# Optimization experiments

Measured on AMD Instinct MI355X. Metric: run time of the kernel, lower is better.

## Reference

```python
import jax, jax.numpy as jnp
import numpy as np

B, N = 4, 65536
Z_DIM, HIDDEN, N_LAYERS = 64, 128, 4
PE_FREQS = 10
FEAT_RES = 16  # global_feat_res
IN_DIM = Z_DIM + 3 + 3 * 2 * PE_FREQS  # latent + pos-encoded coords


def setup_inputs() -> dict:
    key = jax.random.key(0)
    ks = jax.random.split(key, 4 + 2 * N_LAYERS)
    inp = {}
    # xyz in [-1,1]: used directly as grid_sample grid coordinates
    inp['xyz'] = jax.random.uniform(ks[0], (B, N, 3), jnp.float32, -1.0, 1.0)
    inp['local_latents'] = jax.random.normal(ks[1], (B, Z_DIM, FEAT_RES, FEAT_RES), jnp.float32)
    dims = [IN_DIM] + [HIDDEN] * N_LAYERS
    for i in range(N_LAYERS):
        inp[f'W{i}'] = jax.random.normal(ks[2 + i], (dims[i], dims[i + 1]), jnp.float32) / np.sqrt(dims[i]).astype(np.float32)
        inp[f'b{i}'] = jnp.zeros((dims[i + 1],), jnp.float32)
    inp['Wa'] = jax.random.normal(ks[2 + N_LAYERS], (HIDDEN, 1), jnp.float32) / np.sqrt(HIDDEN).astype(np.float32)
    inp['ba'] = jnp.zeros((1,), jnp.float32)
    return inp


def grid_sample_2d(img, grid):
    # torch F.grid_sample: bilinear, align_corners=False, padding_mode='zeros'
    # img [B,C,H,W], grid [B,Hg,Wg,2] in [-1,1], (x,y) order -> out [B,C,Hg,Wg]
    _, _, H, W = img.shape
    x = (grid[..., 0] + 1.0) * (W * 0.5) - 0.5
    y = (grid[..., 1] + 1.0) * (H * 0.5) - 0.5
    x0 = jnp.floor(x); y0 = jnp.floor(y)
    x1 = x0 + 1.0; y1 = y0 + 1.0

    def gather(ix, iy):
        valid = (ix >= 0) & (ix <= W - 1) & (iy >= 0) & (iy <= H - 1)
        ixc = jnp.clip(ix, 0, W - 1).astype(jnp.int32)
        iyc = jnp.clip(iy, 0, H - 1).astype(jnp.int32)
        v = jax.vmap(lambda im, yy, xx: im[:, yy, xx])(img, iyc, ixc)  # [B,C,Hg,Wg]
        return v * valid[:, None].astype(img.dtype)

    out = (gather(x0, y0) * ((x1 - x) * (y1 - y))[:, None]
           + gather(x0, y1) * ((x1 - x) * (y - y0))[:, None]
           + gather(x1, y0) * ((x - x0) * (y1 - y))[:, None]
           + gather(x1, y1) * ((x - x0) * (y - y0))[:, None])
    return out


def positional_encoding(x):
    # x [P,3] -> [P, 3 + 3*2*PE_FREQS]
    freqs = 2.0 ** jnp.arange(PE_FREQS, dtype=x.dtype)
    ang = x[..., None, :] * freqs[:, None]  # [P, L, 3]
    P = x.shape[0]
    return jnp.concatenate([x, jnp.sin(ang).reshape(P, -1), jnp.cos(ang).reshape(P, -1)], axis=-1)


def _forward(xyz, local_latents, Ws, bs, Wa, ba):
    xyz4 = xyz[:, None]  # [B, 1, N, 3] (forward's xyz.unsqueeze(1))
    # sample_local_latents: 4D latents -> grid = xyz[..., [0, 2]]
    grid = jnp.stack([xyz4[..., 0], xyz4[..., 2]], axis=-1)  # [B,1,N,2]
    samp = grid_sample_2d(local_latents, grid)               # [B,C,1,N]
    z = samp.transpose(0, 2, 3, 1).reshape(-1, Z_DIM)        # [B*N, C]
    # get_local_coordinates (preserve_y=True since latents are 4D)
    lc = (xyz4 + 1.0) * 0.5 * FEAT_RES
    lc = lc - jnp.round(lc - 0.5)  # round-half-to-even matches torch .round()
    lc = lc * 2.0 - 1.0
    coords = jnp.concatenate([lc[..., 0:1], xyz4[..., 1:2], lc[..., 2:3]], axis=-1).reshape(-1, 3)
    # local_generator MLP (viewdirs=None on alpha-only path)
    h = jnp.concatenate([z, positional_encoding(coords)], axis=-1)
    for W, b in zip(Ws, bs):
        h = jax.nn.relu(h @ W + b)
    alpha = h @ Wa + ba  # [B*N, 1], raw alpha (activation happens in volume render, not here)
    return alpha.reshape(xyz.shape[0], 1, -1)  # alpha.view(B, n_samples=1, samples_per_ray=N)


def reference(xyz, local_latents, W0, b0, W1, b1, W2, b2, W3, b3, Wa, ba):
    return _forward(xyz, local_latents, (W0, W1, W2, W3), (b0, b1, b2, b3), Wa, ba)
```

## Files before the change

kernel.cpp:

```cpp
#include <hip/hip_runtime.h>
#include <hip/hip_bf16.h>

typedef float f32x4 __attribute__((ext_vector_type(4)));
typedef short bf16x8 __attribute__((ext_vector_type(8)));

__device__ __forceinline__ unsigned pk2(float lo, float hi) {
  union { __hip_bfloat162 h2; unsigned u; } c;
  c.h2 = __float22bfloat162_rn(make_float2(lo, hi));
  return c.u;
}
__device__ __forceinline__ ushort f2bf1(float f) {
  union { __hip_bfloat16 h; ushort u; } c;
  c.h = __float2bfloat16(f);
  return c.u;
}
__device__ __forceinline__ float u2f(unsigned u) {
  union { unsigned u; float f; } c; c.u = u; return c.f;
}

__global__ void pack_all(const float* __restrict__ W0, const float* __restrict__ W1,
                         const float* __restrict__ W2, const float* __restrict__ W3,
                         const float* __restrict__ b0, const float* __restrict__ b1,
                         const float* __restrict__ b2, const float* __restrict__ b3,
                         const float* __restrict__ lat,
                         ushort* __restrict__ wpk, float* __restrict__ biasf,
                         ushort* __restrict__ latpk) {
  int t = blockIdx.x * 256 + threadIdx.x;
  if (t < 8192) {
    int lane = t & 63, kt = (t >> 6) & 3, jt = (t >> 8) & 7, layer = t >> 11;
    const float* W = layer == 0 ? W0 : layer == 1 ? W1 : layer == 2 ? W2 : W3;
    int K = (layer == 0) ? 127 : 128;
    int g = lane >> 4, r = lane & 15;
    bf16x8 pk;
#pragma unroll
    for (int i = 0; i < 8; i++) {
      int k = kt * 32 + 8 * g + i;
      pk[i] = (short)((k < K) ? f2bf1(W[k * 128 + jt * 16 + r]) : (ushort)0);
    }
    *(bf16x8*)(wpk + ((t >> 11) * 32 + (jt * 4 + kt)) * 512 + lane * 8) = pk;
  } else if (t < 16384) {
    int t2 = t - 8192;
    int g = t2 & 7, pix = (t2 >> 3) & 255, b = t2 >> 11;
    uint4 w;
    unsigned* wp = &w.x;
#pragma unroll
    for (int i = 0; i < 4; i++)
      wp[i] = pk2(lat[(b * 64 + 8 * g + 2 * i) * 256 + pix],
                  lat[(b * 64 + 8 * g + 2 * i + 1) * 256 + pix]);
    *(uint4*)((char*)latpk + b * 32768 + pix * 128 + ((16 * g) ^ ((pix & 7) << 4))) = w;
  } else if (t < 16896) {
    int t3 = t - 16384;
    int layer = t3 >> 7, j = t3 & 127;
    const float* b = layer == 0 ? b0 : layer == 1 ? b1 : layer == 2 ? b2 : b3;
    biasf[t3] = b[j];
  }
}

__global__ __launch_bounds__(256, 4) void scene_fwd(
    const float* __restrict__ xyz, const ushort* __restrict__ latpk,
    const ushort* __restrict__ wpk, const float* __restrict__ biasf,
    const float* __restrict__ wa, const float* __restrict__ ba,
    float* __restrict__ out) {
  __shared__ char smem[32768];
  const int tid = threadIdx.x;
  const int wave = tid >> 6, lane = tid & 63;
  const int g = lane >> 4, r = lane & 15;
  const int p0 = blockIdx.x * 128;
  const int batch = blockIdx.x >> 9;

  {
    uint4* dst = (uint4*)smem;
    const uint4* src = (const uint4*)((const char*)latpk + batch * 32768);
#pragma unroll
    for (int i = 0; i < 8; i++) dst[i * 256 + tid] = src[i * 256 + tid];
  }
  __syncthreads();

  const int t2 = tid & 127;
  const int p = p0 + t2;
  const float X = xyz[3 * p + 0], Y = xyz[3 * p + 1], Z = xyz[3 * p + 2];
  uint4 fr[8];
  if (tid < 128) {
    float gx = (X + 1.f) * 8.f - 0.5f;
    float gy = (Z + 1.f) * 8.f - 0.5f;
    float x0f = floorf(gx), y0f = floorf(gy);
    float fx = gx - x0f, fy = gy - y0f;
    int ix0 = (int)x0f, iy0 = (int)y0f;
    int ix1 = ix0 + 1, iy1 = iy0 + 1;
    float vx0 = (ix0 >= 0 && ix0 <= 15) ? 1.f : 0.f;
    float vx1 = (ix1 >= 0 && ix1 <= 15) ? 1.f : 0.f;
    float vy0 = (iy0 >= 0 && iy0 <= 15) ? 1.f : 0.f;
    float vy1 = (iy1 >= 0 && iy1 <= 15) ? 1.f : 0.f;
    int cx0 = min(max(ix0, 0), 15), cx1 = min(max(ix1, 0), 15);
    int cy0 = min(max(iy0, 0), 15), cy1 = min(max(iy1, 0), 15);
    float w00 = (1.f - fx) * (1.f - fy) * vx0 * vy0;
    float w01 = (1.f - fx) * fy * vx0 * vy1;
    float w10 = fx * (1.f - fy) * vx1 * vy0;
    float w11 = fx * fy * vx1 * vy1;
    int px00 = cy0 * 16 + cx0, px01 = cy1 * 16 + cx0;
    int px10 = cy0 * 16 + cx1, px11 = cy1 * 16 + cx1;
    int o00 = px00 * 128, s00 = (px00 & 7) << 4;
    int o01 = px01 * 128, s01 = (px01 & 7) << 4;
    int o10 = px10 * 128, s10 = (px10 & 7) << 4;
    int o11 = px11 * 128, s11 = (px11 & 7) << 4;
#pragma unroll
    for (int gr = 0; gr < 8; gr++) {
      const int off = 16 * gr;
      float f[8];
#pragma unroll
      for (int i = 0; i < 8; i++) f[i] = 0.f;
#pragma unroll
      for (int c = 0; c < 4; c++) {
        const char* ap = smem + (c == 0 ? o00 + (off ^ s00) : c == 1 ? o01 + (off ^ s01)
                               : c == 2 ? o10 + (off ^ s10) : o11 + (off ^ s11));
        const float wc = c == 0 ? w00 : c == 1 ? w01 : c == 2 ? w10 : w11;
        uint4 cv = *(const uint4*)ap;
        const unsigned* u = &cv.x;
#pragma unroll
        for (int q = 0; q < 4; q++) {
          f[2 * q]     += wc * u2f(u[q] << 16);
          f[2 * q + 1] += wc * u2f(u[q] & 0xffff0000u);
        }
      }
      fr[gr].x = pk2(f[0], f[1]); fr[gr].y = pk2(f[2], f[3]);
      fr[gr].z = pk2(f[4], f[5]); fr[gr].w = pk2(f[6], f[7]);
    }
  } else {
    float lcx = (X + 1.f) * 8.f; lcx = lcx - rintf(lcx - 0.5f); lcx = lcx * 2.f - 1.f;
    float lcz = (Z + 1.f) * 8.f; lcz = lcz - rintf(lcz - 0.5f); lcz = lcz * 2.f - 1.f;
    const float c0 = lcx, c1 = Y, c2 = lcz;
#pragma unroll
    for (int gr = 0; gr < 8; gr++) {
      unsigned* wo = &fr[gr].x;
#pragma unroll
      for (int q = 0; q < 4; q++) {
        float e[2];
#pragma unroll
        for (int h = 0; h < 2; h++) {
          const int idx = 8 * gr + 2 * q + h;
          float v;
          if (idx == 0) v = c0;
          else if (idx == 1) v = c1;
          else if (idx == 2) v = c2;
          else if (idx == 63) v = 0.f;
          else if (idx < 33) {
            const int s = idx - 3;
            const int d = s % 3;
            const float cc = d == 0 ? c0 : d == 1 ? c1 : c2;
            v = __sinf(cc * (float)(1 << (s / 3)));
          } else {
            const int s = idx - 33;
            const int d = s % 3;
            const float cc = d == 0 ? c0 : d == 1 ? c1 : c2;
            v = __cosf(cc * (float)(1 << (s / 3)));
          }
          e[h] = v;
        }
        wo[q] = pk2(e[0], e[1]);
      }
    }
  }
  __syncthreads();

  {
    const int tile = t2 >> 6, row = t2 & 63;
    char* rowp = smem + tile * 16384 + row * 256;
    const unsigned swz = (unsigned)((row & 7) << 4);
    const int base = (tid < 128) ? 0 : 128;
#pragma unroll
    for (int gr = 0; gr < 8; gr++)
      *(uint4*)(rowp + (((unsigned)(base + 16 * gr)) ^ swz)) = fr[gr];
  }
  __syncthreads();

  const int tileM = wave >> 1;
  const int jh = wave & 1;
  char* hb = smem + tileM * 16384;
  f32x4 acc[4][4];
#pragma unroll 1
  for (int layer = 0; layer < 4; layer++) {
    const float* bias = biasf + layer * 128;
    const ushort* Aw = wpk + layer * 16384;
#pragma unroll
    for (int jt = 0; jt < 4; jt++) {
      f32x4 bf = *(const f32x4*)(bias + (jh * 4 + jt) * 16 + 4 * g);
#pragma unroll
      for (int pt = 0; pt < 4; pt++) acc[jt][pt] = bf;
    }
#pragma unroll
    for (int kt = 0; kt < 4; kt++) {
      bf16x8 Bf[4];
#pragma unroll
      for (int pt = 0; pt < 4; pt++) {
        const int pr = pt * 16 + r;
        Bf[pt] = *(const bf16x8*)(hb + pr * 256 +
                  (((unsigned)(kt * 64 + 16 * g)) ^ ((unsigned)((pr & 7) << 4))));
      }
#pragma unroll
      for (int jt = 0; jt < 4; jt++) {
        bf16x8 Af = *(const bf16x8*)(Aw + ((jh * 4 + jt) * 4 + kt) * 512 + lane * 8);
#pragma unroll
        for (int pt = 0; pt < 4; pt++)
          acc[jt][pt] = __builtin_amdgcn_mfma_f32_16x16x32_bf16(Af, Bf[pt], acc[jt][pt], 0, 0, 0);
      }
    }
    __syncthreads();
    if (layer < 3) {
#pragma unroll
      for (int jt = 0; jt < 4; jt++) {
#pragma unroll
        for (int pt = 0; pt < 4; pt++) {
          const int pr = pt * 16 + r;
          uint2 w;
          w.x = pk2(fmaxf(acc[jt][pt][0], 0.f), fmaxf(acc[jt][pt][1], 0.f));
          w.y = pk2(fmaxf(acc[jt][pt][2], 0.f), fmaxf(acc[jt][pt][3], 0.f));
          *(uint2*)(hb + pr * 256 +
                    (((unsigned)(32 * (jh * 4 + jt) + 8 * g)) ^ ((unsigned)((pr & 7) << 4)))) = w;
        }
      }
      __syncthreads();
    }
  }

  const float ba0 = ba[0];
  float part[4] = {0.f, 0.f, 0.f, 0.f};
#pragma unroll
  for (int jt = 0; jt < 4; jt++) {
    f32x4 wf = *(const f32x4*)(wa + (jh * 4 + jt) * 16 + 4 * g);
#pragma unroll
    for (int pt = 0; pt < 4; pt++) {
#pragma unroll
      for (int i = 0; i < 4; i++)
        part[pt] += fmaxf(acc[jt][pt][i], 0.f) * wf[i];
    }
  }
  float* scr = (float*)smem;
#pragma unroll
  for (int pt = 0; pt < 4; pt++) {
    float s = part[pt];
    s += __shfl_xor(s, 16, 64);
    s += __shfl_xor(s, 32, 64);
    if (lane < 16) scr[(tileM * 2 + jh) * 64 + pt * 16 + lane] = s;
  }
  __syncthreads();
  if (jh == 0 && lane < 16) {
#pragma unroll
    for (int pt = 0; pt < 4; pt++) {
      const int idx = pt * 16 + lane;
      out[p0 + tileM * 64 + idx] =
          scr[(tileM * 2) * 64 + idx] + scr[(tileM * 2 + 1) * 64 + idx] + ba0;
    }
  }
}

extern "C" void kernel_launch(void* const* d_in, const int* in_sizes, int n_in,
                              void* d_out, int out_size, void* d_ws, size_t ws_size,
                              hipStream_t stream) {
  const float* xyz = (const float*)d_in[0];
  const float* lat = (const float*)d_in[1];
  const float* W0 = (const float*)d_in[2];
  const float* b0 = (const float*)d_in[3];
  const float* W1 = (const float*)d_in[4];
  const float* b1 = (const float*)d_in[5];
  const float* W2 = (const float*)d_in[6];
  const float* b2 = (const float*)d_in[7];
  const float* W3 = (const float*)d_in[8];
  const float* b3 = (const float*)d_in[9];
  const float* wa = (const float*)d_in[10];
  const float* ba = (const float*)d_in[11];
  float* out = (float*)d_out;
  ushort* wpk = (ushort*)d_ws;
  float* biasf = (float*)((char*)d_ws + 131072);
  ushort* latpk = (ushort*)((char*)d_ws + 139264);

  pack_all<<<66, 256, 0, stream>>>(W0, W1, W2, W3, b0, b1, b2, b3, lat,
                                   wpk, biasf, latpk);
  scene_fwd<<<2048, 256, 0, stream>>>(xyz, latpk, wpk, biasf, wa, ba, out);
}
```

Measured before the change: 56.68 us.

## Split MLP work by point rows per wave to drop block barriers

Each wave pair now splits its 64-point tile by point rows (two 16-row groups each) and computes all 128 output features, instead of splitting by output features. Because each wave then reads and writes only its own rows of the activation buffer, the per-layer __syncthreads and the shared-memory reduction of the final alpha dot product are removed, and alpha is written directly. In exchange each wave loads twice as many weight fragments per layer and holds the same number of accumulators. The in-place overwrite of rows is safe only because each row is read and written by the same wave.

```diff
diff --git a/kernel.cpp b/kernel.cpp
--- a/kernel.cpp
+++ b/kernel.cpp
@@ -174,82 +174,70 @@
   __syncthreads();
 
   const int tileM = wave >> 1;
-  const int jh = wave & 1;
+  const int ptb = (wave & 1) * 2;
   char* hb = smem + tileM * 16384;
-  f32x4 acc[4][4];
+  f32x4 acc[8][2];
 #pragma unroll 1
   for (int layer = 0; layer < 4; layer++) {
     const float* bias = biasf + layer * 128;
     const ushort* Aw = wpk + layer * 16384;
 #pragma unroll
-    for (int jt = 0; jt < 4; jt++) {
-      f32x4 bf = *(const f32x4*)(bias + (jh * 4 + jt) * 16 + 4 * g);
-#pragma unroll
-      for (int pt = 0; pt < 4; pt++) acc[jt][pt] = bf;
+    for (int jt = 0; jt < 8; jt++) {
+      f32x4 bf = *(const f32x4*)(bias + jt * 16 + 4 * g);
+#pragma unroll
+      for (int pt = 0; pt < 2; pt++) acc[jt][pt] = bf;
     }
 #pragma unroll
     for (int kt = 0; kt < 4; kt++) {
-      bf16x8 Bf[4];
-#pragma unroll
-      for (int pt = 0; pt < 4; pt++) {
-        const int pr = pt * 16 + r;
+      bf16x8 Bf[2];
+#pragma unroll
+      for (int pt = 0; pt < 2; pt++) {
+        const int pr = (ptb + pt) * 16 + r;
         Bf[pt] = *(const bf16x8*)(hb + pr * 256 +
                   (((unsigned)(kt * 64 + 16 * g)) ^ ((unsigned)((pr & 7) << 4))));
       }
 #pragma unroll
-      for (int jt = 0; jt < 4; jt++) {
-        bf16x8 Af = *(const bf16x8*)(Aw + ((jh * 4 + jt) * 4 + kt) * 512 + lane * 8);
-#pragma unroll
-        for (int pt = 0; pt < 4; pt++)
+      for (int jt = 0; jt < 8; jt++) {
+        bf16x8 Af = *(const bf16x8*)(Aw + (jt * 4 + kt) * 512 + lane * 8);
+#pragma unroll
+        for (int pt = 0; pt < 2; pt++)
           acc[jt][pt] = __builtin_amdgcn_mfma_f32_16x16x32_bf16(Af, Bf[pt], acc[jt][pt], 0, 0, 0);
       }
     }
-    __syncthreads();
     if (layer < 3) {
 #pragma unroll
-      for (int jt = 0; jt < 4; jt++) {
-#pragma unroll
-        for (int pt = 0; pt < 4; pt++) {
-          const int pr = pt * 16 + r;
+      for (int jt = 0; jt < 8; jt++) {
+#pragma unroll
+        for (int pt = 0; pt < 2; pt++) {
+          const int pr = (ptb + pt) * 16 + r;
           uint2 w;
           w.x = pk2(fmaxf(acc[jt][pt][0], 0.f), fmaxf(acc[jt][pt][1], 0.f));
           w.y = pk2(fmaxf(acc[jt][pt][2], 0.f), fmaxf(acc[jt][pt][3], 0.f));
           *(uint2*)(hb + pr * 256 +
-                    (((unsigned)(32 * (jh * 4 + jt) + 8 * g)) ^ ((unsigned)((pr & 7) << 4)))) = w;
+                    (((unsigned)(32 * jt + 8 * g)) ^ ((unsigned)((pr & 7) << 4)))) = w;
         }
       }
-      __syncthreads();
     }
   }
 
   const float ba0 = ba[0];
-  float part[4] = {0.f, 0.f, 0.f, 0.f};
-#pragma unroll
-  for (int jt = 0; jt < 4; jt++) {
-    f32x4 wf = *(const f32x4*)(wa + (jh * 4 + jt) * 16 + 4 * g);
-#pragma unroll
-    for (int pt = 0; pt < 4; pt++) {
+  float part[2] = {0.f, 0.f};
+#pragma unroll
+  for (int jt = 0; jt < 8; jt++) {
+    f32x4 wf = *(const f32x4*)(wa + jt * 16 + 4 * g);
+#pragma unroll
+    for (int pt = 0; pt < 2; pt++) {
 #pragma unroll
       for (int i = 0; i < 4; i++)
         part[pt] += fmaxf(acc[jt][pt][i], 0.f) * wf[i];
     }
   }
-  float* scr = (float*)smem;
-#pragma unroll
-  for (int pt = 0; pt < 4; pt++) {
+#pragma unroll
+  for (int pt = 0; pt < 2; pt++) {
     float s = part[pt];
     s += __shfl_xor(s, 16, 64);
     s += __shfl_xor(s, 32, 64);
-    if (lane < 16) scr[(tileM * 2 + jh) * 64 + pt * 16 + lane] = s;
-  }
-  __syncthreads();
-  if (jh == 0 && lane < 16) {
-#pragma unroll
-    for (int pt = 0; pt < 4; pt++) {
-      const int idx = pt * 16 + lane;
-      out[p0 + tileM * 64 + idx] =
-          scr[(tileM * 2) * 64 + idx] + scr[(tileM * 2 + 1) * 64 + idx] + ba0;
-    }
+    if (lane < 16) out[p0 + tileM * 64 + (ptb + pt) * 16 + lane] = s + ba0;
   }
 }
 
```

Measured after the change: 76.66 us. 1.35x slower.

## Gather latents directly from global memory and drop the shared staging copy

Applied to the files above, without the earlier changes.

Stops copying the per-batch 32KB bf16 latent grid into shared memory. The sampling threads now read their four bilinear corners straight from global/L2, with the swizzle removed from the packed latent layout, and write features directly into the activation tile in LDS. This removes one block-wide copy, two barriers and the fr register array, which lowers register pressure. In exchange the gathers become global loads that are less coalesced. It also wraps the MFMA loop in s_setprio and moves the last-layer barrier to just before the scratch reduction.

```diff
diff --git a/kernel.cpp b/kernel.cpp
--- a/kernel.cpp
+++ b/kernel.cpp
@@ -47,7 +47,7 @@
     for (int i = 0; i < 4; i++)
       wp[i] = pk2(lat[(b * 64 + 8 * g + 2 * i) * 256 + pix],
                   lat[(b * 64 + 8 * g + 2 * i + 1) * 256 + pix]);
-    *(uint4*)((char*)latpk + b * 32768 + pix * 128 + ((16 * g) ^ ((pix & 7) << 4))) = w;
+    *(uint4*)((char*)latpk + b * 32768 + pix * 128 + 16 * g) = w;
   } else if (t < 16896) {
     int t3 = t - 16384;
     int layer = t3 >> 7, j = t3 & 127;
@@ -68,108 +68,93 @@
   const int p0 = blockIdx.x * 128;
   const int batch = blockIdx.x >> 9;
 
-  {
-    uint4* dst = (uint4*)smem;
-    const uint4* src = (const uint4*)((const char*)latpk + batch * 32768);
-#pragma unroll
-    for (int i = 0; i < 8; i++) dst[i * 256 + tid] = src[i * 256 + tid];
-  }
-  __syncthreads();
-
   const int t2 = tid & 127;
   const int p = p0 + t2;
   const float X = xyz[3 * p + 0], Y = xyz[3 * p + 1], Z = xyz[3 * p + 2];
-  uint4 fr[8];
-  if (tid < 128) {
-    float gx = (X + 1.f) * 8.f - 0.5f;
-    float gy = (Z + 1.f) * 8.f - 0.5f;
-    float x0f = floorf(gx), y0f = floorf(gy);
-    float fx = gx - x0f, fy = gy - y0f;
-    int ix0 = (int)x0f, iy0 = (int)y0f;
-    int ix1 = ix0 + 1, iy1 = iy0 + 1;
-    float vx0 = (ix0 >= 0 && ix0 <= 15) ? 1.f : 0.f;
-    float vx1 = (ix1 >= 0 && ix1 <= 15) ? 1.f : 0.f;
-    float vy0 = (iy0 >= 0 && iy0 <= 15) ? 1.f : 0.f;
-    float vy1 = (iy1 >= 0 && iy1 <= 15) ? 1.f : 0.f;
-    int cx0 = min(max(ix0, 0), 15), cx1 = min(max(ix1, 0), 15);
-    int cy0 = min(max(iy0, 0), 15), cy1 = min(max(iy1, 0), 15);
-    float w00 = (1.f - fx) * (1.f - fy) * vx0 * vy0;
-    float w01 = (1.f - fx) * fy * vx0 * vy1;
-    float w10 = fx * (1.f - fy) * vx1 * vy0;
-    float w11 = fx * fy * vx1 * vy1;
-    int px00 = cy0 * 16 + cx0, px01 = cy1 * 16 + cx0;
-    int px10 = cy0 * 16 + cx1, px11 = cy1 * 16 + cx1;
-    int o00 = px00 * 128, s00 = (px00 & 7) << 4;
-    int o01 = px01 * 128, s01 = (px01 & 7) << 4;
-    int o10 = px10 * 128, s10 = (px10 & 7) << 4;
-    int o11 = px11 * 128, s11 = (px11 & 7) << 4;
-#pragma unroll
-    for (int gr = 0; gr < 8; gr++) {
-      const int off = 16 * gr;
-      float f[8];
-#pragma unroll
-      for (int i = 0; i < 8; i++) f[i] = 0.f;
-#pragma unroll
-      for (int c = 0; c < 4; c++) {
-        const char* ap = smem + (c == 0 ? o00 + (off ^ s00) : c == 1 ? o01 + (off ^ s01)
-                               : c == 2 ? o10 + (off ^ s10) : o11 + (off ^ s11));
-        const float wc = c == 0 ? w00 : c == 1 ? w01 : c == 2 ? w10 : w11;
-        uint4 cv = *(const uint4*)ap;
-        const unsigned* u = &cv.x;
-#pragma unroll
-        for (int q = 0; q < 4; q++) {
-          f[2 * q]     += wc * u2f(u[q] << 16);
-          f[2 * q + 1] += wc * u2f(u[q] & 0xffff0000u);
-        }
-      }
-      fr[gr].x = pk2(f[0], f[1]); fr[gr].y = pk2(f[2], f[3]);
-      fr[gr].z = pk2(f[4], f[5]); fr[gr].w = pk2(f[6], f[7]);
-    }
-  } else {
-    float lcx = (X + 1.f) * 8.f; lcx = lcx - rintf(lcx - 0.5f); lcx = lcx * 2.f - 1.f;
-    float lcz = (Z + 1.f) * 8.f; lcz = lcz - rintf(lcz - 0.5f); lcz = lcz * 2.f - 1.f;
-    const float c0 = lcx, c1 = Y, c2 = lcz;
-#pragma unroll
-    for (int gr = 0; gr < 8; gr++) {
-      unsigned* wo = &fr[gr].x;
-#pragma unroll
-      for (int q = 0; q < 4; q++) {
-        float e[2];
-#pragma unroll
-        for (int h = 0; h < 2; h++) {
-          const int idx = 8 * gr + 2 * q + h;
-          float v;
-          if (idx == 0) v = c0;
-          else if (idx == 1) v = c1;
-          else if (idx == 2) v = c2;
-          else if (idx == 63) v = 0.f;
-          else if (idx < 33) {
-            const int s = idx - 3;
-            const int d = s % 3;
-            const float cc = d == 0 ? c0 : d == 1 ? c1 : c2;
-            v = __sinf(cc * (float)(1 << (s / 3)));
-          } else {
-            const int s = idx - 33;
-            const int d = s % 3;
-            const float cc = d == 0 ? c0 : d == 1 ? c1 : c2;
-            v = __cosf(cc * (float)(1 << (s / 3)));
-          }
-          e[h] = v;
-        }
-        wo[q] = pk2(e[0], e[1]);
-      }
-    }
-  }
-  __syncthreads();
-
   {
     const int tile = t2 >> 6, row = t2 & 63;
     char* rowp = smem + tile * 16384 + row * 256;
     const unsigned swz = (unsigned)((row & 7) << 4);
-    const int base = (tid < 128) ? 0 : 128;
-#pragma unroll
-    for (int gr = 0; gr < 8; gr++)
-      *(uint4*)(rowp + (((unsigned)(base + 16 * gr)) ^ swz)) = fr[gr];
+    if (tid < 128) {
+      const char* latb = (const char*)latpk + batch * 32768;
+      float gx = (X + 1.f) * 8.f - 0.5f;
+      float gy = (Z + 1.f) * 8.f - 0.5f;
+      float x0f = floorf(gx), y0f = floorf(gy);
+      float fx = gx - x0f, fy = gy - y0f;
+      int ix0 = (int)x0f, iy0 = (int)y0f;
+      int ix1 = ix0 + 1, iy1 = iy0 + 1;
+      float vx0 = (ix0 >= 0 && ix0 <= 15) ? 1.f : 0.f;
+      float vx1 = (ix1 >= 0 && ix1 <= 15) ? 1.f : 0.f;
+      float vy0 = (iy0 >= 0 && iy0 <= 15) ? 1.f : 0.f;
+      float vy1 = (iy1 >= 0 && iy1 <= 15) ? 1.f : 0.f;
+      int cx0 = min(max(ix0, 0), 15), cx1 = min(max(ix1, 0), 15);
+      int cy0 = min(max(iy0, 0), 15), cy1 = min(max(iy1, 0), 15);
+      float w00 = (1.f - fx) * (1.f - fy) * vx0 * vy0;
+      float w01 = (1.f - fx) * fy * vx0 * vy1;
+      float w10 = fx * (1.f - fy) * vx1 * vy0;
+      float w11 = fx * fy * vx1 * vy1;
+      const char* a00 = latb + (cy0 * 16 + cx0) * 128;
+      const char* a01 = latb + (cy1 * 16 + cx0) * 128;
+      const char* a10 = latb + (cy0 * 16 + cx1) * 128;
+      const char* a11 = latb + (cy1 * 16 + cx1) * 128;
+#pragma unroll 2
+      for (int gr = 0; gr < 8; gr++) {
+        const int off = 16 * gr;
+        uint4 c00 = *(const uint4*)(a00 + off);
+        uint4 c01 = *(const uint4*)(a01 + off);
+        uint4 c10 = *(const uint4*)(a10 + off);
+        uint4 c11 = *(const uint4*)(a11 + off);
+        const unsigned* u00 = &c00.x; const unsigned* u01 = &c01.x;
+        const unsigned* u10 = &c10.x; const unsigned* u11 = &c11.x;
+        uint4 wv;
+        unsigned* wo = &wv.x;
+#pragma unroll
+        for (int q = 0; q < 4; q++) {
+          float lo = w00 * u2f(u00[q] << 16) + w01 * u2f(u01[q] << 16) +
+                     w10 * u2f(u10[q] << 16) + w11 * u2f(u11[q] << 16);
+          float hi = w00 * u2f(u00[q] & 0xffff0000u) + w01 * u2f(u01[q] & 0xffff0000u) +
+                     w10 * u2f(u10[q] & 0xffff0000u) + w11 * u2f(u11[q] & 0xffff0000u);
+          wo[q] = pk2(lo, hi);
+        }
+        *(uint4*)(rowp + (((unsigned)off) ^ swz)) = wv;
+      }
+    } else {
+      float lcx = (X + 1.f) * 8.f; lcx = lcx - rintf(lcx - 0.5f); lcx = lcx * 2.f - 1.f;
+      float lcz = (Z + 1.f) * 8.f; lcz = lcz - rintf(lcz - 0.5f); lcz = lcz * 2.f - 1.f;
+      const float c0 = lcx, c1 = Y, c2 = lcz;
+#pragma unroll
+      for (int gr = 0; gr < 8; gr++) {
+        uint4 wv;
+        unsigned* wo = &wv.x;
+#pragma unroll
+        for (int q = 0; q < 4; q++) {
+          float e[2];
+#pragma unroll
+          for (int h = 0; h < 2; h++) {
+            const int idx = 8 * gr + 2 * q + h;
+            float v;
+            if (idx == 0) v = c0;
+            else if (idx == 1) v = c1;
+            else if (idx == 2) v = c2;
+            else if (idx == 63) v = 0.f;
+            else if (idx < 33) {
+              const int s = idx - 3;
+              const int d = s % 3;
+              const float cc = d == 0 ? c0 : d == 1 ? c1 : c2;
+              v = __sinf(cc * (float)(1 << (s / 3)));
+            } else {
+              const int s = idx - 33;
+              const int d = s % 3;
+              const float cc = d == 0 ? c0 : d == 1 ? c1 : c2;
+              v = __cosf(cc * (float)(1 << (s / 3)));
+            }
+            e[h] = v;
+          }
+          wo[q] = pk2(e[0], e[1]);
+        }
+        *(uint4*)(rowp + (((unsigned)(128 + 16 * gr)) ^ swz)) = wv;
+      }
+    }
   }
   __syncthreads();
 
@@ -196,6 +181,7 @@
         Bf[pt] = *(const bf16x8*)(hb + pr * 256 +
                   (((unsigned)(kt * 64 + 16 * g)) ^ ((unsigned)((pr & 7) << 4))));
       }
+      __builtin_amdgcn_s_setprio(1);
 #pragma unroll
       for (int jt = 0; jt < 4; jt++) {
         bf16x8 Af = *(const bf16x8*)(Aw + ((jh * 4 + jt) * 4 + kt) * 512 + lane * 8);
@@ -203,9 +189,10 @@
         for (int pt = 0; pt < 4; pt++)
           acc[jt][pt] = __builtin_amdgcn_mfma_f32_16x16x32_bf16(Af, Bf[pt], acc[jt][pt], 0, 0, 0);
       }
-    }
-    __syncthreads();
+      __builtin_amdgcn_s_setprio(0);
+    }
     if (layer < 3) {
+      __syncthreads();
 #pragma unroll
       for (int jt = 0; jt < 4; jt++) {
 #pragma unroll
@@ -234,6 +221,7 @@
         part[pt] += fmaxf(acc[jt][pt][i], 0.f) * wf[i];
     }
   }
+  __syncthreads();
   float* scr = (float*)smem;
 #pragma unroll
   for (int pt = 0; pt < 4; pt++) {
```

Result: slower. 60.84 us (+7.3%).
